# Performance work log

Hardware: AMD Instinct MI355X
Metric: run time of the kernel (lower is better)

## Reference

```python
import jax, jax.numpy as jnp
import numpy as np

N_NODES = 50000
N_EDGES = 300000
IN_DIM = 64
EMB = 256
L_OUT = 3   # outer message-passing layers
L_IN = 3    # inner GINConv layers inside each PyG GIN model
BN_EPS = 1e-5


def setup_inputs() -> dict:
    key = jax.random.key(0)
    ks = jax.random.split(key, 8)
    x = jax.random.normal(ks[0], (N_NODES, IN_DIM), dtype=jnp.float32)
    edge_index = jax.random.randint(ks[1], (2, N_EDGES), 0, N_NODES, dtype=jnp.int32)
    Wenc = jax.random.normal(ks[2], (IN_DIM, EMB), dtype=jnp.float32) * 0.05
    benc = jnp.zeros((EMB,), jnp.float32)
    W1 = jax.random.normal(ks[3], (L_OUT, L_IN, EMB, EMB), dtype=jnp.float32) * 0.05
    b1 = jnp.zeros((L_OUT, L_IN, EMB), jnp.float32)
    W2 = jax.random.normal(ks[4], (L_OUT, L_IN, EMB, EMB), dtype=jnp.float32) * 0.05
    b2 = jnp.zeros((L_OUT, L_IN, EMB), jnp.float32)
    gamma = jnp.ones((L_OUT, EMB), jnp.float32)
    beta = jnp.zeros((L_OUT, EMB), jnp.float32)
    return {"x": x, "edge_index": edge_index, "Wenc": Wenc, "benc": benc,
            "W1": W1, "b1": b1, "W2": W2, "b2": b2, "gamma": gamma, "beta": beta}


def reference(x, edge_index, Wenc, benc, W1, b1, W2, b2, gamma, beta):
    src, dst = edge_index[0], edge_index[1]
    h = x @ Wenc + benc                                   # atom encoder [N, EMB]
    for l in range(L_OUT):
        g = h
        for i in range(L_IN):                             # inner GINConvs of PyG GIN model
            agg = jax.ops.segment_sum(g[src], dst, num_segments=N_NODES)
            z = g + agg                                   # (1+eps)*x + sum_neigh, eps=0
            g = jnp.maximum(z @ W1[l, i] + b1[l, i], 0.0) @ W2[l, i] + b2[l, i]
            if i < L_IN - 1:                              # ReLU between inner convs, not after last
                g = jnp.maximum(g, 0.0)
        mean = jnp.mean(g, axis=0)                        # BatchNorm1d, batch stats (biased var)
        var = jnp.var(g, axis=0)
        g = (g - mean) * jax.lax.rsqrt(var + BN_EPS) * gamma[l] + beta[l]
        if l < L_OUT - 1:                                 # ReLU except final layer; dropout = eval identity
            g = jnp.maximum(g, 0.0)
        h = g
    return h                                              # JK='last'
```

## Files before the change

kernel.cpp:

```cpp
#include <hip/hip_runtime.h>
#include <hip/hip_bf16.h>

#define N_NODES 50000
#define N_EDGES 300000
#define IN_DIM 64
#define EMB 256
#define BN_EPS 1e-5f
#define IDX_CAP 1536

typedef _Float16 half8 __attribute__((ext_vector_type(8)));
typedef _Float16 half4 __attribute__((ext_vector_type(4)));
typedef float f32x4 __attribute__((ext_vector_type(4)));

__device__ __forceinline__ f32x4 mfma16(half8 a, half8 b, f32x4 c) {
    return __builtin_amdgcn_mfma_f32_16x16x32_f16(a, b, c, 0, 0, 0);
}

__device__ __forceinline__ void h2f8(half8 v, f32x4& lo, f32x4& hi) {
#pragma unroll
    for (int j = 0; j < 4; j++) { lo[j] = (float)v[j]; hi[j] = (float)v[4 + j]; }
}

__global__ void pack_weights(const float* __restrict__ W1, const float* __restrict__ W2,
                             const float* __restrict__ Wenc, _Float16* __restrict__ wp) {
    int cid = blockIdx.x * 256 + threadIdx.x;
    if (cid < 18 * 8192) {
        int w = cid >> 13;
        int rem = cid & 8191;
        int nt = rem >> 9;
        int ks = (rem >> 6) & 7;
        int lane = rem & 63;
        int li = w >> 1;
        const float* src = ((w & 1) ? W2 : W1) + (size_t)li * EMB * EMB;
        _Float16* dst = wp + (size_t)cid * 8;
        int n = nt * 16 + (lane & 15);
        int kb = ks * 32 + (lane >> 4) * 8;
#pragma unroll
        for (int j = 0; j < 8; j++) dst[j] = (_Float16)src[(kb + j) * EMB + n];
    } else if (cid < 18 * 8192 + 2048) {
        int c = cid - 18 * 8192;
        int nt = c >> 7;
        int ks = (c >> 6) & 1;
        int lane = c & 63;
        _Float16* dst = wp + (size_t)18 * 65536 + (size_t)c * 8;
        int n = nt * 16 + (lane & 15);
        int kb = ks * 32 + (lane >> 4) * 8;
#pragma unroll
        for (int j = 0; j < 8; j++) dst[j] = (_Float16)Wenc[(kb + j) * EMB + n];
    }
}

__global__ void edge_count(const int* __restrict__ dst, unsigned* __restrict__ counts) {
    int e = blockIdx.x * 256 + threadIdx.x;
    if (e < N_EDGES) atomicAdd(&counts[dst[e]], 1u);
}

__global__ void scan_kernel(const unsigned* __restrict__ counts,
                            unsigned* __restrict__ rowptr, unsigned* __restrict__ cursor) {
    __shared__ unsigned wsum[16];
    __shared__ unsigned run;
    int t = threadIdx.x, wv = t >> 6, lane = t & 63;
    if (t == 0) { run = 0; rowptr[0] = 0; }
    __syncthreads();
    for (int base = 0; base < N_NODES; base += 1024) {
        int i = base + t;
        unsigned v = (i < N_NODES) ? counts[i] : 0u;
        unsigned x = v;
#pragma unroll
        for (int off = 1; off < 64; off <<= 1) {
            unsigned y = __shfl_up(x, off, 64);
            if (lane >= off) x += y;
        }
        if (lane == 63) wsum[wv] = x;
        __syncthreads();
        if (wv == 0) {
            unsigned s = (lane < 16) ? wsum[lane] : 0u;
#pragma unroll
            for (int off = 1; off < 16; off <<= 1) {
                unsigned y = __shfl_up(s, off, 64);
                if (lane >= off) s += y;
            }
            if (lane < 16) wsum[lane] = s;
        }
        __syncthreads();
        unsigned waveoff = (wv > 0) ? wsum[wv - 1] : 0u;
        unsigned incl = run + waveoff + x;
        if (i < N_NODES) { rowptr[i + 1] = incl; cursor[i] = incl - v; }
        __syncthreads();
        if (t == 1023) run = incl;
        __syncthreads();
    }
}

__global__ void edge_fill(const int* __restrict__ src, const int* __restrict__ dst,
                          unsigned* __restrict__ cursor, unsigned* __restrict__ csr_src) {
    int e = blockIdx.x * 256 + threadIdx.x;
    if (e < N_EDGES) {
        unsigned pos = atomicAdd(&cursor[dst[e]], 1u);
        csr_src[pos] = (unsigned)src[e];
    }
}

__global__ void __launch_bounds__(256) enc_kernel(const float* __restrict__ x,
                                                  const _Float16* __restrict__ wenc,
                                                  const float* __restrict__ benc,
                                                  _Float16* __restrict__ g) {
    int t = threadIdx.x, w = t >> 6, lane = t & 63;
    int rl = lane & 15, khi = lane >> 4;
    int row0 = blockIdx.x * 64;
    f32x4 acc[4][4];
#pragma unroll
    for (int rf = 0; rf < 4; rf++)
#pragma unroll
        for (int nt = 0; nt < 4; nt++) acc[rf][nt] = (f32x4){0.f, 0.f, 0.f, 0.f};
    const half8* bp = (const half8*)wenc + (size_t)(w * 4) * 128 + lane;
#pragma unroll
    for (int ks = 0; ks < 2; ks++) {
        half8 a[4];
#pragma unroll
        for (int rf = 0; rf < 4; rf++) {
            int n = row0 + rf * 16 + rl;
            f32x4 a0 = (f32x4){0.f,0.f,0.f,0.f}, a1 = (f32x4){0.f,0.f,0.f,0.f};
            if (n < N_NODES) {
                const float* ap = x + (size_t)n * IN_DIM + ks * 32 + khi * 8;
                a0 = *(const f32x4*)ap;
                a1 = *(const f32x4*)(ap + 4);
            }
#pragma unroll
            for (int j = 0; j < 4; j++) { a[rf][j] = (_Float16)a0[j]; a[rf][4 + j] = (_Float16)a1[j]; }
        }
        half8 b[4];
#pragma unroll
        for (int nt = 0; nt < 4; nt++) b[nt] = bp[nt * 128 + ks * 64];
#pragma unroll
        for (int rf = 0; rf < 4; rf++)
#pragma unroll
            for (int nt = 0; nt < 4; nt++) acc[rf][nt] = mfma16(a[rf], b[nt], acc[rf][nt]);
    }
#pragma unroll
    for (int nt = 0; nt < 4; nt++) {
        int col = w * 64 + nt * 16 + rl;
        float bias = benc[col];
#pragma unroll
        for (int rf = 0; rf < 4; rf++)
#pragma unroll
            for (int r = 0; r < 4; r++) {
                int n = row0 + rf * 16 + khi * 4 + r;
                if (n < N_NODES) g[(size_t)n * EMB + col] = (_Float16)(acc[rf][nt][r] + bias);
            }
    }
}

__global__ void __launch_bounds__(256, 4) conv_kernel(
    const _Float16* __restrict__ gin, const unsigned* __restrict__ rowptr,
    const unsigned* __restrict__ csr_src,
    const _Float16* __restrict__ w1p, const float* __restrict__ b1,
    const _Float16* __restrict__ w2p, const float* __restrict__ b2,
    _Float16* __restrict__ gout_h, float* __restrict__ gout_f,
    const float* __restrict__ ssp, float* __restrict__ statp, int relu_out)
{
    __shared__ __align__(16) _Float16 zt[64 * 256];
    __shared__ unsigned lidx[IDX_CAP];
    __shared__ unsigned lrp[68];
    int t = threadIdx.x, w = t >> 6, lane = t & 63;
    int rl = lane & 15, khi = lane >> 4;
    int hw = lane >> 5, hl = lane & 31;
    int row0 = blockIdx.x * 64;

    if (t < 65) {
        int rr = row0 + t;
        lrp[t] = rowptr[rr < N_NODES ? rr : N_NODES];
    }
    __syncthreads();
    unsigned ebase = lrp[0];
    unsigned etot = lrp[64] - ebase;
    unsigned ecnt = etot < IDX_CAP ? etot : IDX_CAP;
    for (unsigned i = t; i < ecnt; i += 256) lidx[i] = csr_src[ebase + i];
    __syncthreads();

    const half8* g8 = (const half8*)gin;
    bool affine = (ssp != nullptr);
    f32x4 scLo = (f32x4){1.f,1.f,1.f,1.f}, scHi = scLo;
    f32x4 shLo = (f32x4){0.f,0.f,0.f,0.f}, shHi = shLo;
    if (affine) {
        scLo = *(const f32x4*)&ssp[hl * 8];
        scHi = *(const f32x4*)&ssp[hl * 8 + 4];
        shLo = *(const f32x4*)&ssp[EMB + hl * 8];
        shHi = *(const f32x4*)&ssp[EMB + hl * 8 + 4];
    }
    auto tvL = [&](f32x4 v) -> f32x4 {
        if (affine) {
#pragma unroll
            for (int j = 0; j < 4; j++) v[j] = fmaxf(v[j] * scLo[j] + shLo[j], 0.f);
        }
        return v;
    };
    auto tvH = [&](f32x4 v) -> f32x4 {
        if (affine) {
#pragma unroll
            for (int j = 0; j < 4; j++) v[j] = fmaxf(v[j] * scHi[j] + shHi[j], 0.f);
        }
        return v;
    };

    int rbase = w * 16 + hw * 8;
    auto do_gather = [&](auto fetch_idx) {
        for (int rr = 0; rr < 8; rr++) {
            int rloc = rbase + rr;
            int n = row0 + rloc;
            f32x4 aLo = (f32x4){0.f,0.f,0.f,0.f}, aHi = (f32x4){0.f,0.f,0.f,0.f};
            if (n < N_NODES) {
                half8 sv = g8[(size_t)n * 32 + hl];
                f32x4 l, h; h2f8(sv, l, h);
                aLo = tvL(l); aHi = tvH(h);
                unsigned beg = lrp[rloc], end = lrp[rloc + 1];
                for (unsigned e = beg; e < end; e += 8) {
                    unsigned last = end - 1;
                    unsigned idx[8];
#pragma unroll
                    for (int j = 0; j < 8; j++) {
                        unsigned ee = e + j; ee = ee < last ? ee : last;
                        idx[j] = fetch_idx(ee);
                    }
                    half8 v[8];
#pragma unroll
                    for (int j = 0; j < 8; j++) v[j] = g8[(size_t)idx[j] * 32 + hl];
#pragma unroll
                    for (int j = 0; j < 8; j++) {
                        float m = (e + j < end) ? 1.f : 0.f;
                        f32x4 vl, vh; h2f8(v[j], vl, vh);
                        aLo += tvL(vl) * m;
                        aHi += tvH(vh) * m;
                    }
                }
            }
            half8 hz;
#pragma unroll
            for (int j = 0; j < 4; j++) { hz[j] = (_Float16)aLo[j]; hz[4 + j] = (_Float16)aHi[j]; }
            *(half8*)&zt[rloc * 256 + ((hl * 8) ^ ((rloc & 15) << 3))] = hz;
        }
    };
    if (etot <= IDX_CAP) do_gather([&](unsigned ee) { return lidx[ee - ebase]; });
    else                 do_gather([&](unsigned ee) { return csr_src[ee]; });
    __syncthreads();

    f32x4 acc1[4][4];
#pragma unroll
    for (int rf = 0; rf < 4; rf++)
#pragma unroll
        for (int nt = 0; nt < 4; nt++) acc1[rf][nt] = (f32x4){0.f, 0.f, 0.f, 0.f};
    {
        const half8* bp = (const half8*)w1p + (size_t)(w * 4) * 512 + lane;
#pragma unroll
        for (int ks = 0; ks < 8; ks++) {
            half8 a[4];
#pragma unroll
            for (int rf = 0; rf < 4; rf++) {
                int row = rf * 16 + rl;
                a[rf] = *(const half8*)&zt[row * 256 + ((ks * 32 + khi * 8) ^ ((row & 15) << 3))];
            }
            half8 b[4];
#pragma unroll
            for (int nt = 0; nt < 4; nt++) b[nt] = bp[nt * 512 + ks * 64];
#pragma unroll
            for (int rf = 0; rf < 4; rf++)
#pragma unroll
                for (int nt = 0; nt < 4; nt++) acc1[rf][nt] = mfma16(a[rf], b[nt], acc1[rf][nt]);
        }
    }
    __syncthreads();
#pragma unroll
    for (int nt = 0; nt < 4; nt++) {
        int col = w * 64 + nt * 16 + rl;
        float bias = b1[col];
#pragma unroll
        for (int rf = 0; rf < 4; rf++)
#pragma unroll
            for (int r = 0; r < 4; r++) {
                int row = rf * 16 + khi * 4 + r;
                float v = fmaxf(acc1[rf][nt][r] + bias, 0.f);
                zt[row * 256 + (col ^ ((row & 15) << 3))] = (_Float16)v;
            }
    }
    __syncthreads();

    f32x4 acc2[4][4];
#pragma unroll
    for (int rf = 0; rf < 4; rf++)
#pragma unroll
        for (int nt = 0; nt < 4; nt++) acc2[rf][nt] = (f32x4){0.f, 0.f, 0.f, 0.f};
    {
        const half8* bp = (const half8*)w2p + (size_t)(w * 4) * 512 + lane;
#pragma unroll
        for (int ks = 0; ks < 8; ks++) {
            half8 a[4];
#pragma unroll
            for (int rf = 0; rf < 4; rf++) {
                int row = rf * 16 + rl;
                a[rf] = *(const half8*)&zt[row * 256 + ((ks * 32 + khi * 8) ^ ((row & 15) << 3))];
            }
            half8 b[4];
#pragma unroll
            for (int nt = 0; nt < 4; nt++) b[nt] = bp[nt * 512 + ks * 64];
#pragma unroll
            for (int rf = 0; rf < 4; rf++)
#pragma unroll
                for (int nt = 0; nt < 4; nt++) acc2[rf][nt] = mfma16(a[rf], b[nt], acc2[rf][nt]);
        }
    }
    bool wf = (gout_f != nullptr);
#pragma unroll
    for (int nt = 0; nt < 4; nt++) {
        int col = w * 64 + nt * 16 + rl;
        float bias = b2[col];
        float sS = 0.f, s2S = 0.f;
#pragma unroll
        for (int rf = 0; rf < 4; rf++)
#pragma unroll
            for (int r = 0; r < 4; r++) {
                int row = rf * 16 + khi * 4 + r;
                int n = row0 + row;
                float v = acc2[rf][nt][r] + bias;
                if (relu_out) v = fmaxf(v, 0.f);
                if (n < N_NODES) {
                    if (wf) gout_f[(size_t)n * EMB + col] = v;
                    else    gout_h[(size_t)n * EMB + col] = (_Float16)v;
                    sS += v; s2S += v * v;
                }
            }
        if (statp) {
            sS += __shfl_xor(sS, 16); s2S += __shfl_xor(s2S, 16);
            sS += __shfl_xor(sS, 32); s2S += __shfl_xor(s2S, 32);
            if (khi == 0) {
                atomicAdd(&statp[col], sS);
                atomicAdd(&statp[EMB + col], s2S);
            }
        }
    }
}

__global__ void bn_finalize(const float* __restrict__ stats, const float* __restrict__ gamma,
                            const float* __restrict__ beta, float* __restrict__ ss) {
    int c = threadIdx.x;
    float mean = stats[c] * (1.f / N_NODES);
    float var = stats[EMB + c] * (1.f / N_NODES) - mean * mean;
    float scale = gamma[c] * rsqrtf(var + BN_EPS);
    ss[c] = scale;
    ss[EMB + c] = beta[c] - mean * scale;
}

__global__ void bn_apply(const float* __restrict__ gin, const float* __restrict__ ss,
                         float* __restrict__ gout) {
    int i = blockIdx.x * 256 + threadIdx.x;
    if (i >= N_NODES * 64) return;
    int c4 = (i & 63) * 4;
    f32x4 v = ((const f32x4*)gin)[i];
    f32x4 sc = *(const f32x4*)&ss[c4];
    f32x4 sh = *(const f32x4*)&ss[EMB + c4];
    f32x4 r;
#pragma unroll
    for (int j = 0; j < 4; j++) r[j] = v[j] * sc[j] + sh[j];
    ((f32x4*)gout)[i] = r;
}

extern "C" void kernel_launch(void* const* d_in, const int* in_sizes, int n_in,
                              void* d_out, int out_size, void* d_ws, size_t ws_size,
                              hipStream_t stream) {
    const float* x     = (const float*)d_in[0];
    const int*   ei    = (const int*)d_in[1];
    const float* Wenc  = (const float*)d_in[2];
    const float* benc  = (const float*)d_in[3];
    const float* W1    = (const float*)d_in[4];
    const float* b1    = (const float*)d_in[5];
    const float* W2    = (const float*)d_in[6];
    const float* b2    = (const float*)d_in[7];
    const float* gamma = (const float*)d_in[8];
    const float* beta  = (const float*)d_in[9];
    float* out = (float*)d_out;

    char* p = (char*)d_ws;
    auto alloc = [&](size_t bytes) { void* q = (void*)p; p += (bytes + 255) & ~(size_t)255; return q; };
    _Float16*  gh0     = (_Float16*)alloc((size_t)N_NODES * EMB * 2);
    _Float16*  gh1     = (_Float16*)alloc((size_t)N_NODES * EMB * 2);
    _Float16*  wp      = (_Float16*)alloc((size_t)(18 * 65536 + 16384) * 2);
    unsigned*  counts  = (unsigned*)alloc((size_t)N_NODES * 4);
    unsigned*  rowptr  = (unsigned*)alloc((size_t)(N_NODES + 1) * 4);
    unsigned*  cursor  = (unsigned*)alloc((size_t)N_NODES * 4);
    unsigned*  csr_src = (unsigned*)alloc((size_t)N_EDGES * 4);
    float*     stats   = (float*)alloc(3 * 512 * 4);
    float*     ss      = (float*)alloc(3 * 512 * 4);

    hipMemsetAsync(counts, 0, (size_t)N_NODES * 4, stream);
    hipMemsetAsync(stats, 0, 3 * 512 * 4, stream);
    pack_weights<<<584, 256, 0, stream>>>(W1, W2, Wenc, wp);
    edge_count<<<(N_EDGES + 255) / 256, 256, 0, stream>>>(ei + N_EDGES, counts);
    scan_kernel<<<1, 1024, 0, stream>>>(counts, rowptr, cursor);
    edge_fill<<<(N_EDGES + 255) / 256, 256, 0, stream>>>(ei, ei + N_EDGES, cursor, csr_src);

    enc_kernel<<<782, 256, 0, stream>>>(x, wp + (size_t)18 * 65536, benc, gh0);

    _Float16* cur = gh0;
    _Float16* nxt = gh1;
    for (int l = 0; l < 3; l++) {
        for (int i = 0; i < 3; i++) {
            int li = l * 3 + i;
            bool last = (l == 2 && i == 2);
            const float* ssp = (i == 0 && l > 0) ? (ss + (size_t)(l - 1) * 512) : nullptr;
            float* statp = (i == 2) ? (stats + (size_t)l * 512) : nullptr;
            conv_kernel<<<782, 256, 0, stream>>>(
                cur, rowptr, csr_src,
                wp + (size_t)(li * 2) * 65536, b1 + li * EMB,
                wp + (size_t)(li * 2 + 1) * 65536, b2 + li * EMB,
                last ? nullptr : nxt, last ? out : nullptr,
                ssp, statp, (i < 2) ? 1 : 0);
            if (!last) { _Float16* tmp = cur; cur = nxt; nxt = tmp; }
        }
        bn_finalize<<<1, 256, 0, stream>>>(stats + (size_t)l * 512, gamma + l * EMB,
                                           beta + l * EMB, ss + (size_t)l * 512);
    }
    bn_apply<<<(N_NODES * 64 + 255) / 256, 256, 0, stream>>>(out, ss + 2 * 512, out);
}
```

Before: 756.9 us.

## Split fused conv kernel into separate gather and MLP kernels

Splits the fused gather+MLP conv kernel into two launches. A fine-grained gather kernel assigns one node per 32 lanes across many small blocks and writes the aggregated fp16 features to a workspace buffer. A separate MLP kernel loads that buffer into LDS and runs the MFMA GEMMs. This is meant to fix load imbalance and low occupancy in the fused gather phase, at the cost of an extra global write and read of the N x 256 fp16 buffer per conv plus an extra launch. The MLP kernel writes its output in place into the same buffer the gather read, which is safe only because the kernels are ordered on one stream.

```diff
diff --git a/kernel.cpp b/kernel.cpp
--- a/kernel.cpp
+++ b/kernel.cpp
@@ -6,10 +6,8 @@
 #define IN_DIM 64
 #define EMB 256
 #define BN_EPS 1e-5f
-#define IDX_CAP 1536
 
 typedef _Float16 half8 __attribute__((ext_vector_type(8)));
-typedef _Float16 half4 __attribute__((ext_vector_type(4)));
 typedef float f32x4 __attribute__((ext_vector_type(4)));
 
 __device__ __forceinline__ f32x4 mfma16(half8 a, half8 b, f32x4 c) {
@@ -151,34 +149,16 @@
     }
 }
 
-__global__ void __launch_bounds__(256, 4) conv_kernel(
+__global__ void __launch_bounds__(256) gather_kernel(
     const _Float16* __restrict__ gin, const unsigned* __restrict__ rowptr,
-    const unsigned* __restrict__ csr_src,
-    const _Float16* __restrict__ w1p, const float* __restrict__ b1,
-    const _Float16* __restrict__ w2p, const float* __restrict__ b2,
-    _Float16* __restrict__ gout_h, float* __restrict__ gout_f,
-    const float* __restrict__ ssp, float* __restrict__ statp, int relu_out)
+    const unsigned* __restrict__ csr_src, const float* __restrict__ ssp,
+    _Float16* __restrict__ zout)
 {
-    __shared__ __align__(16) _Float16 zt[64 * 256];
-    __shared__ unsigned lidx[IDX_CAP];
-    __shared__ unsigned lrp[68];
-    int t = threadIdx.x, w = t >> 6, lane = t & 63;
-    int rl = lane & 15, khi = lane >> 4;
-    int hw = lane >> 5, hl = lane & 31;
-    int row0 = blockIdx.x * 64;
-
-    if (t < 65) {
-        int rr = row0 + t;
-        lrp[t] = rowptr[rr < N_NODES ? rr : N_NODES];
-    }
-    __syncthreads();
-    unsigned ebase = lrp[0];
-    unsigned etot = lrp[64] - ebase;
-    unsigned ecnt = etot < IDX_CAP ? etot : IDX_CAP;
-    for (unsigned i = t; i < ecnt; i += 256) lidx[i] = csr_src[ebase + i];
-    __syncthreads();
-
+    int n = blockIdx.x * 8 + (threadIdx.x >> 5);
+    int hl = threadIdx.x & 31;
+    if (n >= N_NODES) return;
     const half8* g8 = (const half8*)gin;
+
     bool affine = (ssp != nullptr);
     f32x4 scLo = (f32x4){1.f,1.f,1.f,1.f}, scHi = scLo;
     f32x4 shLo = (f32x4){0.f,0.f,0.f,0.f}, shHi = shLo;
@@ -203,45 +183,60 @@
         return v;
     };
 
-    int rbase = w * 16 + hw * 8;
-    auto do_gather = [&](auto fetch_idx) {
-        for (int rr = 0; rr < 8; rr++) {
-            int rloc = rbase + rr;
-            int n = row0 + rloc;
-            f32x4 aLo = (f32x4){0.f,0.f,0.f,0.f}, aHi = (f32x4){0.f,0.f,0.f,0.f};
-            if (n < N_NODES) {
-                half8 sv = g8[(size_t)n * 32 + hl];
-                f32x4 l, h; h2f8(sv, l, h);
-                aLo = tvL(l); aHi = tvH(h);
-                unsigned beg = lrp[rloc], end = lrp[rloc + 1];
-                for (unsigned e = beg; e < end; e += 8) {
-                    unsigned last = end - 1;
-                    unsigned idx[8];
-#pragma unroll
-                    for (int j = 0; j < 8; j++) {
-                        unsigned ee = e + j; ee = ee < last ? ee : last;
-                        idx[j] = fetch_idx(ee);
-                    }
-                    half8 v[8];
-#pragma unroll
-                    for (int j = 0; j < 8; j++) v[j] = g8[(size_t)idx[j] * 32 + hl];
-#pragma unroll
-                    for (int j = 0; j < 8; j++) {
-                        float m = (e + j < end) ? 1.f : 0.f;
-                        f32x4 vl, vh; h2f8(v[j], vl, vh);
-                        aLo += tvL(vl) * m;
-                        aHi += tvH(vh) * m;
-                    }
-                }
-            }
-            half8 hz;
-#pragma unroll
-            for (int j = 0; j < 4; j++) { hz[j] = (_Float16)aLo[j]; hz[4 + j] = (_Float16)aHi[j]; }
-            *(half8*)&zt[rloc * 256 + ((hl * 8) ^ ((rloc & 15) << 3))] = hz;
-        }
-    };
-    if (etot <= IDX_CAP) do_gather([&](unsigned ee) { return lidx[ee - ebase]; });
-    else                 do_gather([&](unsigned ee) { return csr_src[ee]; });
+    half8 sv = g8[(size_t)n * 32 + hl];
+    f32x4 l0, h0; h2f8(sv, l0, h0);
+    f32x4 aLo = tvL(l0), aHi = tvH(h0);
+
+    unsigned beg = rowptr[n], end = rowptr[n + 1];
+    for (unsigned e = beg; e < end; e += 8) {
+        unsigned last = end - 1;
+        unsigned idx[8];
+#pragma unroll
+        for (int j = 0; j < 8; j++) {
+            unsigned ee = e + j; ee = ee < last ? ee : last;
+            idx[j] = csr_src[ee];
+        }
+        half8 v[8];
+#pragma unroll
+        for (int j = 0; j < 8; j++) v[j] = g8[(size_t)idx[j] * 32 + hl];
+#pragma unroll
+        for (int j = 0; j < 8; j++) {
+            float m = (e + j < end) ? 1.f : 0.f;
+            f32x4 vl, vh; h2f8(v[j], vl, vh);
+            aLo += tvL(vl) * m;
+            aHi += tvH(vh) * m;
+        }
+    }
+    half8 hz;
+#pragma unroll
+    for (int j = 0; j < 4; j++) { hz[j] = (_Float16)aLo[j]; hz[4 + j] = (_Float16)aHi[j]; }
+    ((half8*)zout)[(size_t)n * 32 + hl] = hz;
+}
+
+__global__ void __launch_bounds__(256) mlp_kernel(
+    const _Float16* __restrict__ z,
+    const _Float16* __restrict__ w1p, const float* __restrict__ b1,
+    const _Float16* __restrict__ w2p, const float* __restrict__ b2,
+    _Float16* __restrict__ gout_h, float* __restrict__ gout_f,
+    float* __restrict__ statp, int relu_out)
+{
+    __shared__ __align__(16) _Float16 zt[64 * 256];
+    int t = threadIdx.x, w = t >> 6, lane = t & 63;
+    int rl = lane & 15, khi = lane >> 4;
+    int row0 = blockIdx.x * 64;
+
+    {
+        int rrow = t >> 5, c8 = t & 31;
+        const half8* z8 = (const half8*)z;
+#pragma unroll
+        for (int p = 0; p < 8; p++) {
+            int row = p * 8 + rrow;
+            int n = row0 + row;
+            half8 v = (half8){0,0,0,0,0,0,0,0};
+            if (n < N_NODES) v = z8[(size_t)n * 32 + c8];
+            *(half8*)&zt[row * 256 + ((c8 * 8) ^ ((row & 15) << 3))] = v;
+        }
+    }
     __syncthreads();
 
     f32x4 acc1[4][4];
@@ -380,8 +375,8 @@
 
     char* p = (char*)d_ws;
     auto alloc = [&](size_t bytes) { void* q = (void*)p; p += (bytes + 255) & ~(size_t)255; return q; };
-    _Float16*  gh0     = (_Float16*)alloc((size_t)N_NODES * EMB * 2);
-    _Float16*  gh1     = (_Float16*)alloc((size_t)N_NODES * EMB * 2);
+    _Float16*  gh      = (_Float16*)alloc((size_t)N_NODES * EMB * 2);
+    _Float16*  zh      = (_Float16*)alloc((size_t)N_NODES * EMB * 2);
     _Float16*  wp      = (_Float16*)alloc((size_t)(18 * 65536 + 16384) * 2);
     unsigned*  counts  = (unsigned*)alloc((size_t)N_NODES * 4);
     unsigned*  rowptr  = (unsigned*)alloc((size_t)(N_NODES + 1) * 4);
@@ -397,23 +392,21 @@
     scan_kernel<<<1, 1024, 0, stream>>>(counts, rowptr, cursor);
     edge_fill<<<(N_EDGES + 255) / 256, 256, 0, stream>>>(ei, ei + N_EDGES, cursor, csr_src);
 
-    enc_kernel<<<782, 256, 0, stream>>>(x, wp + (size_t)18 * 65536, benc, gh0);
-
-    _Float16* cur = gh0;
-    _Float16* nxt = gh1;
+    enc_kernel<<<782, 256, 0, stream>>>(x, wp + (size_t)18 * 65536, benc, gh);
+
+    const int ggrid = (N_NODES + 7) / 8;
     for (int l = 0; l < 3; l++) {
         for (int i = 0; i < 3; i++) {
             int li = l * 3 + i;
             bool last = (l == 2 && i == 2);
             const float* ssp = (i == 0 && l > 0) ? (ss + (size_t)(l - 1) * 512) : nullptr;
             float* statp = (i == 2) ? (stats + (size_t)l * 512) : nullptr;
-            conv_kernel<<<782, 256, 0, stream>>>(
-                cur, rowptr, csr_src,
-                wp + (size_t)(li * 2) * 65536, b1 + li * EMB,
+            gather_kernel<<<ggrid, 256, 0, stream>>>(gh, rowptr, csr_src, ssp, zh);
+            mlp_kernel<<<782, 256, 0, stream>>>(
+                zh, wp + (size_t)(li * 2) * 65536, b1 + li * EMB,
                 wp + (size_t)(li * 2 + 1) * 65536, b2 + li * EMB,
-                last ? nullptr : nxt, last ? out : nullptr,
-                ssp, statp, (i < 2) ? 1 : 0);
-            if (!last) { _Float16* tmp = cur; cur = nxt; nxt = tmp; }
+                last ? nullptr : gh, last ? out : nullptr,
+                statp, (i < 2) ? 1 : 0);
         }
         bn_finalize<<<1, 256, 0, stream>>>(stats + (size_t)l * 512, gamma + l * EMB,
                                            beta + l * EMB, ss + (size_t)l * 512);
```

New measurement: 926.0 us. 1.22x slower.
